# Kernel optimization log

Measured on AMD Instinct MI355X. Metric: run time of the kernel, lower is better.

The kernel has to match this reference:

```python
import jax, jax.numpy as jnp
import numpy as np

B, D_IN, H = 32768, 256, 128
N_TASK, N_EXP, N_SHARE = 2, 4, 4


def setup_inputs() -> dict:
    key = jax.random.key(0)
    ks = jax.random.split(key, 4)
    s = 1.0 / np.sqrt(D_IN)
    return {
        "x": jax.random.normal(ks[0], (B, D_IN), dtype=jnp.float32),
        "W_share": jax.random.normal(ks[1], (N_SHARE, D_IN, H), dtype=jnp.float32) * s,
        "b_share": jnp.zeros((N_SHARE, H), dtype=jnp.float32),
        "W_task": jax.random.normal(ks[2], (N_TASK, N_EXP, D_IN, H), dtype=jnp.float32) * s,
        "b_task": jnp.zeros((N_TASK, N_EXP, H), dtype=jnp.float32),
        "W_gate": jax.random.normal(ks[3], (N_TASK, D_IN, N_SHARE + N_EXP), dtype=jnp.float32) * s,
        "b_gate": jnp.zeros((N_TASK, N_SHARE + N_EXP), dtype=jnp.float32),
    }


def reference(x, W_share, b_share, W_task, b_task, W_gate, b_gate):
    # shared experts: [B, N_SHARE, H]
    share = jax.nn.relu(jnp.einsum('bd,edh->beh', x, W_share) + b_share)
    # task-specific experts: [T, B, N_EXP, H]
    task = jax.nn.relu(jnp.einsum('bd,tedh->tbeh', x, W_task) + b_task[:, None])
    # gates: [T, B, N_SHARE + N_EXP], softmax over experts
    gate = jax.nn.softmax(jnp.einsum('bd,tdg->tbg', x, W_gate) + b_gate[:, None], axis=-1)
    # concat order matches original: share_net first, then task experts
    share_b = jnp.broadcast_to(share[None], (N_TASK, B, N_SHARE, H))
    experts = jnp.concatenate([share_b, task], axis=2)  # [T, B, N_SHARE+N_EXP, H]
    towers = jnp.einsum('tbeh,tbe->tbh', experts, gate)  # [T, B, H]
    return towers
```

## Files before the change

### kernel.cpp

```cpp
#include <hip/hip_runtime.h>


typedef __attribute__((ext_vector_type(8))) short short8;
typedef __attribute__((ext_vector_type(4))) float float4v;

#define WF_GOFF_US 393216
#define WS_NEED_B  802816

__device__ __forceinline__ unsigned short f2bf(float f) {
  unsigned u = __builtin_bit_cast(unsigned, f);
  u += 0x7FFFu + ((u >> 16) & 1u);
  return (unsigned short)(u >> 16);
}

__device__ __forceinline__ int slot2e(int sr, int t) {
  return (sr < 4) ? sr : 4 + t * 4 + (sr - 4);
}

__global__ __launch_bounds__(256)
void prep_kernel(const float* __restrict__ Ws,
                 const float* __restrict__ Wt,
                 const float* __restrict__ Wg,
                 unsigned short* __restrict__ WT) {
  int bid = blockIdx.x;
  int tid = threadIdx.x;
  if (bid < 96) {
    int e = bid >> 3, h16 = bid & 7;
    const float* src = (e < 4) ? Ws + ((size_t)e << 15)
                               : Wt + ((size_t)(e - 4) << 15);
    int k = tid;
    int kk = k >> 5, quad = (k >> 3) & 3, j = k & 7;
    size_t eb = ((size_t)(e * 8 + h16) * 8 + kk) * 512 + (size_t)quad * 128 + j;
    const float* sp = src + (size_t)k * 128 + h16 * 16;
    #pragma unroll
    for (int c4 = 0; c4 < 4; ++c4) {
      float4 v = *(const float4*)(sp + c4 * 4);
      WT[eb + (size_t)(c4 * 4 + 0) * 8] = f2bf(v.x);
      WT[eb + (size_t)(c4 * 4 + 1) * 8] = f2bf(v.y);
      WT[eb + (size_t)(c4 * 4 + 2) * 8] = f2bf(v.z);
      WT[eb + (size_t)(c4 * 4 + 3) * 8] = f2bf(v.w);
    }
  } else {
    #pragma unroll
    for (int it = 0; it < 16; ++it) {
      int jj = it * 256 + tid;
      int n = jj >> 8, k = jj & 255;
      int tt = n >> 3, g = n & 7;
      WT[WF_GOFF_US + jj] = f2bf(Wg[(size_t)(tt * 256 + k) * 8 + g]);
    }
  }
}

__global__ __launch_bounds__(256)
void dmoe_main(const float* __restrict__ x,
               const unsigned short* __restrict__ WT,
               const float* __restrict__ b_share,
               const float* __restrict__ b_task,
               const float* __restrict__ b_gate,
               float* __restrict__ out) {
  __shared__ float gw[4][8][20];

  const int tid  = threadIdx.x;
  const int lane = tid & 63;
  const int w    = tid >> 6;
  const int col  = lane & 15;
  const int quad = lane >> 4;
  const int blk  = blockIdx.x;
  const int t    = blk & 1;
  const int hh   = (blk >> 1) & 1;
  const int rg   = blk >> 2;
  const int h16  = hh * 4 + w;
  const int h0   = h16 * 16;

  short8 wf[8][8];
  #pragma unroll
  for (int sr = 0; sr < 8; ++sr) {
    const int e = slot2e(sr, t);
    const unsigned short* p = WT + ((size_t)(e * 8 + h16) * 8) * 512
                            + (size_t)lane * 8;
    #pragma unroll
    for (int kk = 0; kk < 8; ++kk) {
      wf[sr][kk] = *(const short8*)(p + (size_t)kk * 512);
      asm volatile("" : "+a"(wf[sr][kk]));
    }
  }

  short8 Bg[8];
  {
    const unsigned short* bp = WT + WF_GOFF_US
                             + (size_t)(t * 8 + (col & 7)) * 256 + quad * 8;
    #pragma unroll
    for (int kk = 0; kk < 8; ++kk) Bg[kk] = *(const short8*)(bp + kk * 32);
  }
  const float bg = b_gate[t * 8 + (col & 7)];

  float bias_r[8];
  #pragma unroll
  for (int sr = 0; sr < 8; ++sr)
    bias_r[sr] = (sr < 4) ? b_share[sr * 128 + h0 + col]
                          : b_task[(size_t)(t * 4 + (sr - 4)) * 128 + h0 + col];

  const float* xb = x + ((size_t)rg * 512 + col) * 256 + quad * 8;
  float* ob = out + ((size_t)t << 22)
            + ((size_t)rg * 512 + quad * 4) * 128 + h0 + col;

  uint4 pr[16];
  #pragma unroll
  for (int ks = 0; ks < 8; ++ks) {
    pr[2 * ks]     = *(const uint4*)(xb + ks * 32);
    pr[2 * ks + 1] = *(const uint4*)(xb + ks * 32 + 4);
  }

  #pragma unroll 1
  for (int mi = 0; mi < 32; ++mi) {
    short8 A[8];
    #pragma unroll
    for (int ks = 0; ks < 8; ++ks) {
      float4v u = __builtin_bit_cast(float4v, pr[2 * ks]);
      float4v v = __builtin_bit_cast(float4v, pr[2 * ks + 1]);
      short8 fr;
      fr[0] = (short)f2bf(u[0]); fr[1] = (short)f2bf(u[1]);
      fr[2] = (short)f2bf(u[2]); fr[3] = (short)f2bf(u[3]);
      fr[4] = (short)f2bf(v[0]); fr[5] = (short)f2bf(v[1]);
      fr[6] = (short)f2bf(v[2]); fr[7] = (short)f2bf(v[3]);
      A[ks] = fr;
    }
    if (mi < 31) {
      const float* xn = xb + (size_t)(mi + 1) * (16 * 256);
      #pragma unroll
      for (int ks = 0; ks < 8; ++ks) {
        pr[2 * ks]     = *(const uint4*)(xn + ks * 32);
        pr[2 * ks + 1] = *(const uint4*)(xn + ks * 32 + 4);
      }
    }

    float4v acc[8];
    #pragma unroll
    for (int i = 0; i < 8; ++i) acc[i] = (float4v){0.f, 0.f, 0.f, 0.f};

    float4v ag = {0.f, 0.f, 0.f, 0.f};
    #pragma unroll
    for (int ks = 0; ks < 8; ++ks) {
      ag     = __builtin_amdgcn_mfma_f32_16x16x32_bf16(A[ks], Bg[ks],     ag,     0, 0, 0);
      acc[0] = __builtin_amdgcn_mfma_f32_16x16x32_bf16(A[ks], wf[0][ks], acc[0], 0, 0, 0);
      acc[1] = __builtin_amdgcn_mfma_f32_16x16x32_bf16(A[ks], wf[1][ks], acc[1], 0, 0, 0);
      acc[2] = __builtin_amdgcn_mfma_f32_16x16x32_bf16(A[ks], wf[2][ks], acc[2], 0, 0, 0);
      acc[3] = __builtin_amdgcn_mfma_f32_16x16x32_bf16(A[ks], wf[3][ks], acc[3], 0, 0, 0);
    }

    {
      float ps[4];
      #pragma unroll
      for (int r = 0; r < 4; ++r) {
        float vlog = ag[r] + bg;
        float m = vlog;
        m = fmaxf(m, __shfl_xor(m, 1));
        m = fmaxf(m, __shfl_xor(m, 2));
        m = fmaxf(m, __shfl_xor(m, 4));
        float pe = __expf(vlog - m);
        float ss = pe;
        ss += __shfl_xor(ss, 1);
        ss += __shfl_xor(ss, 2);
        ss += __shfl_xor(ss, 4);
        ps[r] = pe / ss;
      }
      if (col < 8) {
        float4 gv = {ps[0], ps[1], ps[2], ps[3]};
        *(float4*)&gw[w][col][quad * 4] = gv;
      }
    }

    #pragma unroll
    for (int ks = 0; ks < 8; ++ks) {
      acc[4] = __builtin_amdgcn_mfma_f32_16x16x32_bf16(A[ks], wf[4][ks], acc[4], 0, 0, 0);
      acc[5] = __builtin_amdgcn_mfma_f32_16x16x32_bf16(A[ks], wf[5][ks], acc[5], 0, 0, 0);
      acc[6] = __builtin_amdgcn_mfma_f32_16x16x32_bf16(A[ks], wf[6][ks], acc[6], 0, 0, 0);
      acc[7] = __builtin_amdgcn_mfma_f32_16x16x32_bf16(A[ks], wf[7][ks], acc[7], 0, 0, 0);
    }

    float ow[4] = {0.f, 0.f, 0.f, 0.f};
    #pragma unroll
    for (int sr = 0; sr < 8; ++sr) {
      float4 gv = *(const float4*)&gw[w][sr][quad * 4];
      #pragma unroll
      for (int r = 0; r < 4; ++r) {
        float vv = fmaxf(acc[sr][r] + bias_r[sr], 0.f);
        ow[r] += ((const float*)&gv)[r] * vv;
      }
    }
    float* op = ob + (size_t)mi * (16 * 128);
    #pragma unroll
    for (int r = 0; r < 4; ++r)
      __builtin_nontemporal_store(ow[r], op + r * 128);
  }
}

extern "C" void kernel_launch(void* const* d_in, const int* in_sizes, int n_in,
                              void* d_out, int out_size, void* d_ws, size_t ws_size,
                              hipStream_t stream) {
  const float* x       = (const float*)d_in[0];
  const float* W_share = (const float*)d_in[1];
  const float* b_share = (const float*)d_in[2];
  const float* W_task  = (const float*)d_in[3];
  const float* b_task  = (const float*)d_in[4];
  const float* W_gate  = (const float*)d_in[5];
  const float* b_gate  = (const float*)d_in[6];
  float* out = (float*)d_out;
  unsigned short* WT = (unsigned short*)d_ws;

  prep_kernel<<<97, 256, 0, stream>>>(W_share, W_task, W_gate, WT);
  dmoe_main<<<256, 256, 0, stream>>>(x, WT, b_share, b_task, b_gate, out);
}
```

Baseline: 172.9 us.

## Split K across two waves per block with LDS partial-sum exchange

Blocks shrink to two waves, each owning half of the 256-wide K dimension for one 16-column H slice. The register-resident weight fragments per wave drop to half, which allows two blocks per CU and a grid of 1024 blocks. Partial accumulators and gate logits are exchanged through LDS, and the finishing role alternates between the waves each row tile. The cost is a __syncthreads and the LDS traffic for nine float4 vectors per tile, and x is now read by eight blocks per row group instead of two.

```diff
diff --git a/kernel.cpp b/kernel.cpp
--- a/kernel.cpp
+++ b/kernel.cpp
@@ -51,14 +51,16 @@
   }
 }
 
-__global__ __launch_bounds__(256)
+__global__ __launch_bounds__(128, 2)
 void dmoe_main(const float* __restrict__ x,
                const unsigned short* __restrict__ WT,
                const float* __restrict__ b_share,
                const float* __restrict__ b_task,
                const float* __restrict__ b_gate,
                float* __restrict__ out) {
-  __shared__ float gw[4][8][20];
+  __shared__ float exch[2][9][64][4];
+  __shared__ float gw[2][8][20];
+  __shared__ float biasL[8][16];
 
   const int tid  = threadIdx.x;
   const int lane = tid & 63;
@@ -67,55 +69,55 @@
   const int quad = lane >> 4;
   const int blk  = blockIdx.x;
   const int t    = blk & 1;
-  const int hh   = (blk >> 1) & 1;
-  const int rg   = blk >> 2;
-  const int h16  = hh * 4 + w;
+  const int h16  = (blk >> 1) & 7;
+  const int rg   = blk >> 4;
   const int h0   = h16 * 16;
 
-  short8 wf[8][8];
+  const float* xb = x + ((size_t)rg * 512 + col) * 256 + w * 128 + quad * 8;
+  uint4 pr[8];
+  #pragma unroll
+  for (int ks = 0; ks < 4; ++ks) {
+    pr[2 * ks]     = *(const uint4*)(xb + ks * 32);
+    pr[2 * ks + 1] = *(const uint4*)(xb + ks * 32 + 4);
+  }
+
+  short8 wf[8][4];
   #pragma unroll
   for (int sr = 0; sr < 8; ++sr) {
     const int e = slot2e(sr, t);
-    const unsigned short* p = WT + ((size_t)(e * 8 + h16) * 8) * 512
+    const unsigned short* p = WT + ((size_t)(e * 8 + h16) * 8 + w * 4) * 512
                             + (size_t)lane * 8;
     #pragma unroll
-    for (int kk = 0; kk < 8; ++kk) {
-      wf[sr][kk] = *(const short8*)(p + (size_t)kk * 512);
-      asm volatile("" : "+a"(wf[sr][kk]));
-    }
-  }
-
-  short8 Bg[8];
+    for (int ks = 0; ks < 4; ++ks) {
+      wf[sr][ks] = *(const short8*)(p + (size_t)ks * 512);
+      asm volatile("" : "+a"(wf[sr][ks]));
+    }
+  }
+
+  short8 Bg[4];
   {
     const unsigned short* bp = WT + WF_GOFF_US
-                             + (size_t)(t * 8 + (col & 7)) * 256 + quad * 8;
-    #pragma unroll
-    for (int kk = 0; kk < 8; ++kk) Bg[kk] = *(const short8*)(bp + kk * 32);
+                             + (size_t)(t * 8 + (col & 7)) * 256
+                             + (w * 4) * 32 + quad * 8;
+    #pragma unroll
+    for (int ks = 0; ks < 4; ++ks) Bg[ks] = *(const short8*)(bp + ks * 32);
   }
   const float bg = b_gate[t * 8 + (col & 7)];
 
-  float bias_r[8];
-  #pragma unroll
-  for (int sr = 0; sr < 8; ++sr)
-    bias_r[sr] = (sr < 4) ? b_share[sr * 128 + h0 + col]
-                          : b_task[(size_t)(t * 4 + (sr - 4)) * 128 + h0 + col];
-
-  const float* xb = x + ((size_t)rg * 512 + col) * 256 + quad * 8;
+  {
+    int sr = tid >> 4, c = tid & 15;
+    biasL[sr][c] = (sr < 4) ? b_share[sr * 128 + h0 + c]
+                            : b_task[(size_t)(t * 4 + (sr - 4)) * 128 + h0 + c];
+  }
+
   float* ob = out + ((size_t)t << 22)
             + ((size_t)rg * 512 + quad * 4) * 128 + h0 + col;
 
-  uint4 pr[16];
-  #pragma unroll
-  for (int ks = 0; ks < 8; ++ks) {
-    pr[2 * ks]     = *(const uint4*)(xb + ks * 32);
-    pr[2 * ks + 1] = *(const uint4*)(xb + ks * 32 + 4);
-  }
-
   #pragma unroll 1
   for (int mi = 0; mi < 32; ++mi) {
-    short8 A[8];
-    #pragma unroll
-    for (int ks = 0; ks < 8; ++ks) {
+    short8 A[4];
+    #pragma unroll
+    for (int ks = 0; ks < 4; ++ks) {
       float4v u = __builtin_bit_cast(float4v, pr[2 * ks]);
       float4v v = __builtin_bit_cast(float4v, pr[2 * ks + 1]);
       short8 fr;
@@ -128,7 +130,7 @@
     if (mi < 31) {
       const float* xn = xb + (size_t)(mi + 1) * (16 * 256);
       #pragma unroll
-      for (int ks = 0; ks < 8; ++ks) {
+      for (int ks = 0; ks < 4; ++ks) {
         pr[2 * ks]     = *(const uint4*)(xn + ks * 32);
         pr[2 * ks + 1] = *(const uint4*)(xn + ks * 32 + 4);
       }
@@ -137,18 +139,38 @@
     float4v acc[8];
     #pragma unroll
     for (int i = 0; i < 8; ++i) acc[i] = (float4v){0.f, 0.f, 0.f, 0.f};
-
     float4v ag = {0.f, 0.f, 0.f, 0.f};
     #pragma unroll
-    for (int ks = 0; ks < 8; ++ks) {
+    for (int ks = 0; ks < 4; ++ks) {
       ag     = __builtin_amdgcn_mfma_f32_16x16x32_bf16(A[ks], Bg[ks],     ag,     0, 0, 0);
       acc[0] = __builtin_amdgcn_mfma_f32_16x16x32_bf16(A[ks], wf[0][ks], acc[0], 0, 0, 0);
       acc[1] = __builtin_amdgcn_mfma_f32_16x16x32_bf16(A[ks], wf[1][ks], acc[1], 0, 0, 0);
       acc[2] = __builtin_amdgcn_mfma_f32_16x16x32_bf16(A[ks], wf[2][ks], acc[2], 0, 0, 0);
       acc[3] = __builtin_amdgcn_mfma_f32_16x16x32_bf16(A[ks], wf[3][ks], acc[3], 0, 0, 0);
-    }
-
-    {
+      acc[4] = __builtin_amdgcn_mfma_f32_16x16x32_bf16(A[ks], wf[4][ks], acc[4], 0, 0, 0);
+      acc[5] = __builtin_amdgcn_mfma_f32_16x16x32_bf16(A[ks], wf[5][ks], acc[5], 0, 0, 0);
+      acc[6] = __builtin_amdgcn_mfma_f32_16x16x32_bf16(A[ks], wf[6][ks], acc[6], 0, 0, 0);
+      acc[7] = __builtin_amdgcn_mfma_f32_16x16x32_bf16(A[ks], wf[7][ks], acc[7], 0, 0, 0);
+    }
+
+    const int bi = mi & 1;
+    if (((mi & 1) ^ w) != 0) {
+      *(float4v*)&exch[bi][8][lane][0] = ag;
+      #pragma unroll
+      for (int sr = 0; sr < 8; ++sr)
+        *(float4v*)&exch[bi][sr][lane][0] = acc[sr];
+      __syncthreads();
+    } else {
+      __syncthreads();
+      {
+        float4v o = *(const float4v*)&exch[bi][8][lane][0];
+        ag += o;
+      }
+      #pragma unroll
+      for (int sr = 0; sr < 8; ++sr) {
+        float4v o = *(const float4v*)&exch[bi][sr][lane][0];
+        acc[sr] += o;
+      }
       float ps[4];
       #pragma unroll
       for (int r = 0; r < 4; ++r) {
@@ -166,32 +188,24 @@
       }
       if (col < 8) {
         float4 gv = {ps[0], ps[1], ps[2], ps[3]};
-        *(float4*)&gw[w][col][quad * 4] = gv;
-      }
-    }
-
-    #pragma unroll
-    for (int ks = 0; ks < 8; ++ks) {
-      acc[4] = __builtin_amdgcn_mfma_f32_16x16x32_bf16(A[ks], wf[4][ks], acc[4], 0, 0, 0);
-      acc[5] = __builtin_amdgcn_mfma_f32_16x16x32_bf16(A[ks], wf[5][ks], acc[5], 0, 0, 0);
-      acc[6] = __builtin_amdgcn_mfma_f32_16x16x32_bf16(A[ks], wf[6][ks], acc[6], 0, 0, 0);
-      acc[7] = __builtin_amdgcn_mfma_f32_16x16x32_bf16(A[ks], wf[7][ks], acc[7], 0, 0, 0);
-    }
-
-    float ow[4] = {0.f, 0.f, 0.f, 0.f};
-    #pragma unroll
-    for (int sr = 0; sr < 8; ++sr) {
-      float4 gv = *(const float4*)&gw[w][sr][quad * 4];
-      #pragma unroll
-      for (int r = 0; r < 4; ++r) {
-        float vv = fmaxf(acc[sr][r] + bias_r[sr], 0.f);
-        ow[r] += ((const float*)&gv)[r] * vv;
-      }
-    }
-    float* op = ob + (size_t)mi * (16 * 128);
-    #pragma unroll
-    for (int r = 0; r < 4; ++r)
-      __builtin_nontemporal_store(ow[r], op + r * 128);
+        *(float4*)&gw[bi][col][quad * 4] = gv;
+      }
+      float ow[4] = {0.f, 0.f, 0.f, 0.f};
+      #pragma unroll
+      for (int sr = 0; sr < 8; ++sr) {
+        float4 gv = *(const float4*)&gw[bi][sr][quad * 4];
+        float bias = biasL[sr][col];
+        #pragma unroll
+        for (int r = 0; r < 4; ++r) {
+          float vv = fmaxf(acc[sr][r] + bias, 0.f);
+          ow[r] += ((const float*)&gv)[r] * vv;
+        }
+      }
+      float* op = ob + (size_t)mi * (16 * 128);
+      #pragma unroll
+      for (int r = 0; r < 4; ++r)
+        __builtin_nontemporal_store(ow[r], op + r * 128);
+    }
   }
 }
 
@@ -209,5 +223,5 @@
   unsigned short* WT = (unsigned short*)d_ws;
 
   prep_kernel<<<97, 256, 0, stream>>>(W_share, W_task, W_gate, WT);
-  dmoe_main<<<256, 256, 0, stream>>>(x, WT, b_share, b_task, b_gate, out);
-}
+  dmoe_main<<<1024, 128, 0, stream>>>(x, WT, b_share, b_task, b_gate, out);
+}
```

Result: slower. 283.4 us (+63.9%).
